# Optimization experiments

Hardware: AMD Instinct MI355X
Metric: run time of the kernel (lower is better)

## Reference

```python
import jax, jax.numpy as jnp
import numpy as np

B, S, IN, OUT, E, K = 4, 4096, 1024, 1024, 8, 2
SCALE = 512.0  # alpha / r = 512 / 1
TEMP = 1.0


def setup_inputs() -> dict:
    key = jax.random.key(0)
    k1, k2, k3, k4 = jax.random.split(key, 4)
    return {
        "x": jax.random.normal(k1, (B, S, IN), dtype=jnp.float32),
        "lora_A": jax.random.normal(k2, (E, 1, IN), dtype=jnp.float32) * 0.02,
        "lora_B": jax.random.normal(k3, (E, OUT, 1), dtype=jnp.float32) * 0.02,
        "gate_w": jax.random.normal(k4, (E, IN), dtype=jnp.float32) * 0.02,
        "gate_b": jnp.zeros((E,), dtype=jnp.float32),
    }


def reference(x, lora_A, lora_B, gate_w, gate_b):
    # segment-level gating: mean over seq, softmax over experts
    seg = x.mean(axis=1)                                    # [B, IN]
    logits = (seg @ gate_w.T + gate_b) / TEMP               # [B, E]
    gate_scores = jax.nn.softmax(logits, axis=-1)           # [B, E]
    topk_scores, topk_idx = jax.lax.top_k(gate_scores, K)   # [B, K] (same for all tokens in segment)

    # dense all-expert LoRA compute (eval mode: dropout is identity)
    h = jnp.einsum('bsi,eri->bser', x, lora_A)              # [B, S, E, r]
    expert_outputs = jnp.einsum('bser,eor->bseo', h, lora_B) * SCALE  # [B, S, E, OUT]

    # gather top-k experts per segment (broadcast over seq) and weighted-sum
    sel = jnp.take_along_axis(expert_outputs, topk_idx[:, None, :, None], axis=2)  # [B, S, K, OUT]
    out = jnp.sum(sel * topk_scores[:, None, :, None], axis=2)  # [B, S, OUT]
    return out
```

## Files before the change

### kernel.cpp

```cpp
#include <hip/hip_runtime.h>

#define SCALE_F 512.0f

#define WS_H     0
#define WS_GPART 131072

__global__ __launch_bounds__(256) void kA_h_gate(
    const float* __restrict__ x, const float* __restrict__ lora_A,
    const float* __restrict__ gate_w, float* __restrict__ h,
    float* __restrict__ gpart)
{
    const int tid  = threadIdx.x;
    const int w    = tid >> 6;
    const int lane = tid & 63;
    const int tok0 = blockIdx.x * 8;

    __shared__ float xbuf[8 * 1024];

    float4 W[4][4];
#pragma unroll
    for (int rr = 0; rr < 4; ++rr) {
        const int row = 4 * w + rr;
        const float* rp = (row < 8) ? (lora_A + row * 1024)
                                    : (gate_w + (row - 8) * 1024);
        const float4* rp4 = (const float4*)rp;
#pragma unroll
        for (int j = 0; j < 4; ++j) W[rr][j] = rp4[lane + 64 * j];
    }

    const float4* src = (const float4*)(x + (size_t)tok0 * 1024);
    float4* dst = (float4*)xbuf;
#pragma unroll
    for (int j = 0; j < 8; ++j) dst[tid + 256 * j] = src[tid + 256 * j];
    __syncthreads();

    float gacc[4] = {0.f, 0.f, 0.f, 0.f};

#pragma unroll 2
    for (int t = 0; t < 8; ++t) {
        const float4* xr = (const float4*)(xbuf + t * 1024);
        const float4 xv0 = xr[lane];
        const float4 xv1 = xr[lane + 64];
        const float4 xv2 = xr[lane + 128];
        const float4 xv3 = xr[lane + 192];

        float p[4];
#pragma unroll
        for (int rr = 0; rr < 4; ++rr) {
            const float4 a0 = W[rr][0], a1 = W[rr][1];
            const float4 a2 = W[rr][2], a3 = W[rr][3];
            float s;
            s  = xv0.x * a0.x + xv0.y * a0.y + xv0.z * a0.z + xv0.w * a0.w;
            s += xv1.x * a1.x + xv1.y * a1.y + xv1.z * a1.z + xv1.w * a1.w;
            s += xv2.x * a2.x + xv2.y * a2.y + xv2.z * a2.z + xv2.w * a2.w;
            s += xv3.x * a3.x + xv3.y * a3.y + xv3.z * a3.z + xv3.w * a3.w;
            p[rr] = s;
        }

        if (w < 2) {
#pragma unroll
            for (int off = 32; off > 0; off >>= 1) {
                p[0] += __shfl_xor(p[0], off);
                p[1] += __shfl_xor(p[1], off);
                p[2] += __shfl_xor(p[2], off);
                p[3] += __shfl_xor(p[3], off);
            }
            if (lane == 0) {
                float4 hv = make_float4(p[0], p[1], p[2], p[3]);
                *(float4*)(h + (size_t)(tok0 + t) * 8 + w * 4) = hv;
            }
        } else {
            gacc[0] += p[0]; gacc[1] += p[1]; gacc[2] += p[2]; gacc[3] += p[3];
        }
    }

    if (w >= 2) {
#pragma unroll
        for (int off = 32; off > 0; off >>= 1) {
            gacc[0] += __shfl_xor(gacc[0], off);
            gacc[1] += __shfl_xor(gacc[1], off);
            gacc[2] += __shfl_xor(gacc[2], off);
            gacc[3] += __shfl_xor(gacc[3], off);
        }
        if (lane == 0) {
            float4 gv = make_float4(gacc[0], gacc[1], gacc[2], gacc[3]);
            *(float4*)(gpart + (size_t)blockIdx.x * 8 + (w - 2) * 4) = gv;
        }
    }
}

static __device__ __forceinline__ float4 f4add(float4 a, float4 b) {
    return make_float4(a.x + b.x, a.y + b.y, a.z + b.z, a.w + b.w);
}

__global__ __launch_bounds__(256) void kB_gate_combine(
    const float* __restrict__ h, const float* __restrict__ gpart,
    const float* __restrict__ gate_b, const float* __restrict__ lora_B,
    float* __restrict__ out)
{
    const int tid  = threadIdx.x;
    const int blk  = blockIdx.x;
    const int b    = blk >> 9;
    const int tok0 = blk * 8;

    __shared__ float4 s4[256];
    __shared__ float  s_h[64];
    __shared__ float  s_logit[8];
    __shared__ int    s_sel[2];
    __shared__ float  s_coef[2];

    const float4* gp4 = (const float4*)(gpart + (size_t)b * 4096);
    float4 acc = gp4[tid];
    acc = f4add(acc, gp4[tid + 256]);
    acc = f4add(acc, gp4[tid + 512]);
    acc = f4add(acc, gp4[tid + 768]);
    s4[tid] = acc;

    if (tid < 64) s_h[tid] = h[(size_t)tok0 * 8 + tid];
    __syncthreads();

    if (tid < 64) {
        float4 a = f4add(f4add(s4[tid], s4[tid + 64]),
                         f4add(s4[tid + 128], s4[tid + 192]));
        s4[tid] = a;
    }
    __syncthreads();
    if (tid < 16) {
        float4 a = f4add(f4add(s4[tid], s4[tid + 16]),
                         f4add(s4[tid + 32], s4[tid + 48]));
        s4[tid] = a;
    }
    __syncthreads();
    if (tid < 2) {
        float4 a = s4[tid];
#pragma unroll
        for (int q = 2; q < 16; q += 2) a = f4add(a, s4[tid + q]);
        const float inv = 1.0f / 4096.0f;
        s_logit[tid * 4 + 0] = a.x * inv + gate_b[tid * 4 + 0];
        s_logit[tid * 4 + 1] = a.y * inv + gate_b[tid * 4 + 1];
        s_logit[tid * 4 + 2] = a.z * inv + gate_b[tid * 4 + 2];
        s_logit[tid * 4 + 3] = a.w * inv + gate_b[tid * 4 + 3];
    }
    __syncthreads();

    if (tid == 0) {
        float sc[8];
        float m = -1e30f;
#pragma unroll
        for (int q = 0; q < 8; ++q) { sc[q] = s_logit[q]; m = fmaxf(m, sc[q]); }
        float sum = 0.f;
#pragma unroll
        for (int q = 0; q < 8; ++q) { sc[q] = __expf(sc[q] - m); sum += sc[q]; }
        const float invs = 1.0f / sum;

        int i0 = 0;
#pragma unroll
        for (int q = 1; q < 8; ++q) if (sc[q] > sc[i0]) i0 = q;
        int i1 = (i0 == 0) ? 1 : 0;
#pragma unroll
        for (int q = 0; q < 8; ++q) if (q != i0 && sc[q] > sc[i1]) i1 = q;

        s_sel[0]  = i0;
        s_sel[1]  = i1;
        s_coef[0] = SCALE_F * sc[i0] * invs;
        s_coef[1] = SCALE_F * sc[i1] * invs;
    }
    __syncthreads();

    const int   i0 = s_sel[0];
    const int   i1 = s_sel[1];
    const float c0 = s_coef[0];
    const float c1 = s_coef[1];

    const float4 b0 = ((const float4*)(lora_B + i0 * 1024))[tid];
    const float4 b1 = ((const float4*)(lora_B + i1 * 1024))[tid];
    const float4 v0 = make_float4(c0 * b0.x, c0 * b0.y, c0 * b0.z, c0 * b0.w);
    const float4 v1 = make_float4(c1 * b1.x, c1 * b1.y, c1 * b1.z, c1 * b1.w);

    float4* out4 = (float4*)out;
#pragma unroll
    for (int t = 0; t < 8; ++t) {
        const float h0 = s_h[t * 8 + i0];
        const float h1 = s_h[t * 8 + i1];
        float4 r;
        r.x = h0 * v0.x + h1 * v1.x;
        r.y = h0 * v0.y + h1 * v1.y;
        r.z = h0 * v0.z + h1 * v1.z;
        r.w = h0 * v0.w + h1 * v1.w;
        out4[(size_t)(tok0 + t) * 256 + tid] = r;
    }
}

extern "C" void kernel_launch(void* const* d_in, const int* in_sizes, int n_in,
                              void* d_out, int out_size, void* d_ws, size_t ws_size,
                              hipStream_t stream) {
    const float* x      = (const float*)d_in[0];
    const float* lora_A = (const float*)d_in[1];
    const float* lora_B = (const float*)d_in[2];
    const float* gate_w = (const float*)d_in[3];
    const float* gate_b = (const float*)d_in[4];
    float* out = (float*)d_out;

    float* ws    = (float*)d_ws;
    float* h     = ws + WS_H;
    float* gpart = ws + WS_GPART;

    kA_h_gate<<<2048, 256, 0, stream>>>(x, lora_A, gate_w, h, gpart);
    kB_gate_combine<<<2048, 256, 0, stream>>>(h, gpart, gate_b, lora_B, out);
}
```

Measured before the change: 128.7 us.

## Fuse gating and combine into one cooperative kernel with grid sync

Merges the two kernels into one cooperative kernel of 1024 blocks, each handling two 8-token tiles. The per-token h values stay in shared memory and are never written to global memory. A grid-wide sync separates the gate-partial phase from the softmax/top-k/output phase. This removes one kernel launch and the h round trip, but adds the cost of a grid barrier and needs every block co-resident. If the cooperative launch fails, the code falls back to the original two kernels.

```diff
diff --git a/kernel.cpp b/kernel.cpp
--- a/kernel.cpp
+++ b/kernel.cpp
@@ -1,9 +1,202 @@
 #include <hip/hip_runtime.h>
+#include <hip/hip_cooperative_groups.h>
+
+namespace cg = cooperative_groups;
 
 #define SCALE_F 512.0f
 
 #define WS_H     0
 #define WS_GPART 131072
+
+static __device__ __forceinline__ float4 f4add(float4 a, float4 b) {
+    return make_float4(a.x + b.x, a.y + b.y, a.z + b.z, a.w + b.w);
+}
+
+__global__ __launch_bounds__(256, 4) void k_fused(
+    const float* __restrict__ x, const float* __restrict__ lora_A,
+    const float* __restrict__ gate_w, const float* __restrict__ gate_b,
+    const float* __restrict__ lora_B, float* __restrict__ gpart,
+    float* __restrict__ out)
+{
+    const int tid  = threadIdx.x;
+    const int w    = tid >> 6;
+    const int lane = tid & 63;
+
+    __shared__ __align__(16) float xbuf[8 * 1024];
+    __shared__ __align__(16) float s_h[2][64];
+    __shared__ float4 s4[256];
+    __shared__ float  s_logit[8];
+    __shared__ int    s_sel[2];
+    __shared__ float  s_coef[2];
+
+    float4 W[4][4];
+#pragma unroll
+    for (int rr = 0; rr < 4; ++rr) {
+        const int row = 4 * w + rr;
+        const float* rp = (row < 8) ? (lora_A + row * 1024)
+                                    : (gate_w + (row - 8) * 1024);
+        const float4* rp4 = (const float4*)rp;
+#pragma unroll
+        for (int j = 0; j < 4; ++j) W[rr][j] = rp4[lane + 64 * j];
+    }
+
+#pragma unroll
+    for (int ti = 0; ti < 2; ++ti) {
+        const int tile = blockIdx.x + ti * 1024;
+        const int tok0 = tile * 8;
+
+        if (ti) __syncthreads();
+
+        const float4* src = (const float4*)(x + (size_t)tok0 * 1024);
+        float4* dst = (float4*)xbuf;
+#pragma unroll
+        for (int j = 0; j < 8; ++j) dst[tid + 256 * j] = src[tid + 256 * j];
+        __syncthreads();
+
+        float gacc[4] = {0.f, 0.f, 0.f, 0.f};
+
+#pragma unroll 2
+        for (int t = 0; t < 8; ++t) {
+            const float4* xr = (const float4*)(xbuf + t * 1024);
+            const float4 xv0 = xr[lane];
+            const float4 xv1 = xr[lane + 64];
+            const float4 xv2 = xr[lane + 128];
+            const float4 xv3 = xr[lane + 192];
+
+            float p[4];
+#pragma unroll
+            for (int rr = 0; rr < 4; ++rr) {
+                const float4 a0 = W[rr][0], a1 = W[rr][1];
+                const float4 a2 = W[rr][2], a3 = W[rr][3];
+                float s;
+                s  = xv0.x * a0.x + xv0.y * a0.y + xv0.z * a0.z + xv0.w * a0.w;
+                s += xv1.x * a1.x + xv1.y * a1.y + xv1.z * a1.z + xv1.w * a1.w;
+                s += xv2.x * a2.x + xv2.y * a2.y + xv2.z * a2.z + xv2.w * a2.w;
+                s += xv3.x * a3.x + xv3.y * a3.y + xv3.z * a3.z + xv3.w * a3.w;
+                p[rr] = s;
+            }
+
+            if (w < 2) {
+#pragma unroll
+                for (int off = 32; off > 0; off >>= 1) {
+                    p[0] += __shfl_xor(p[0], off);
+                    p[1] += __shfl_xor(p[1], off);
+                    p[2] += __shfl_xor(p[2], off);
+                    p[3] += __shfl_xor(p[3], off);
+                }
+                if (lane == 0) {
+                    float4 hv = make_float4(p[0], p[1], p[2], p[3]);
+                    *(float4*)&s_h[ti][t * 8 + w * 4] = hv;
+                }
+            } else {
+                gacc[0] += p[0]; gacc[1] += p[1]; gacc[2] += p[2]; gacc[3] += p[3];
+            }
+        }
+
+        if (w >= 2) {
+#pragma unroll
+            for (int off = 32; off > 0; off >>= 1) {
+                gacc[0] += __shfl_xor(gacc[0], off);
+                gacc[1] += __shfl_xor(gacc[1], off);
+                gacc[2] += __shfl_xor(gacc[2], off);
+                gacc[3] += __shfl_xor(gacc[3], off);
+            }
+            if (lane == 0) {
+                float4 gv = make_float4(gacc[0], gacc[1], gacc[2], gacc[3]);
+                *(float4*)(gpart + (size_t)tile * 8 + (w - 2) * 4) = gv;
+            }
+        }
+    }
+
+    __threadfence();
+    cg::this_grid().sync();
+
+#pragma unroll
+    for (int ti = 0; ti < 2; ++ti) {
+        const int tile = blockIdx.x + ti * 1024;
+        const int tok0 = tile * 8;
+        const int b    = tile >> 9;
+
+        if (ti) __syncthreads();
+
+        const float4* gp4 = (const float4*)(gpart + (size_t)b * 4096);
+        float4 acc = gp4[tid];
+        acc = f4add(acc, gp4[tid + 256]);
+        acc = f4add(acc, gp4[tid + 512]);
+        acc = f4add(acc, gp4[tid + 768]);
+        s4[tid] = acc;
+        __syncthreads();
+
+        if (tid < 64) {
+            s4[tid] = f4add(f4add(s4[tid], s4[tid + 64]),
+                            f4add(s4[tid + 128], s4[tid + 192]));
+        }
+        __syncthreads();
+        if (tid < 16) {
+            s4[tid] = f4add(f4add(s4[tid], s4[tid + 16]),
+                            f4add(s4[tid + 32], s4[tid + 48]));
+        }
+        __syncthreads();
+        if (tid < 2) {
+            float4 a = s4[tid];
+#pragma unroll
+            for (int q = 2; q < 16; q += 2) a = f4add(a, s4[tid + q]);
+            const float inv = 1.0f / 4096.0f;
+            s_logit[tid * 4 + 0] = a.x * inv + gate_b[tid * 4 + 0];
+            s_logit[tid * 4 + 1] = a.y * inv + gate_b[tid * 4 + 1];
+            s_logit[tid * 4 + 2] = a.z * inv + gate_b[tid * 4 + 2];
+            s_logit[tid * 4 + 3] = a.w * inv + gate_b[tid * 4 + 3];
+        }
+        __syncthreads();
+
+        if (tid == 0) {
+            float sc[8];
+            float m = -1e30f;
+#pragma unroll
+            for (int q = 0; q < 8; ++q) { sc[q] = s_logit[q]; m = fmaxf(m, sc[q]); }
+            float sum = 0.f;
+#pragma unroll
+            for (int q = 0; q < 8; ++q) { sc[q] = __expf(sc[q] - m); sum += sc[q]; }
+            const float invs = 1.0f / sum;
+
+            int i0 = 0;
+#pragma unroll
+            for (int q = 1; q < 8; ++q) if (sc[q] > sc[i0]) i0 = q;
+            int i1 = (i0 == 0) ? 1 : 0;
+#pragma unroll
+            for (int q = 0; q < 8; ++q) if (q != i0 && sc[q] > sc[i1]) i1 = q;
+
+            s_sel[0]  = i0;
+            s_sel[1]  = i1;
+            s_coef[0] = SCALE_F * sc[i0] * invs;
+            s_coef[1] = SCALE_F * sc[i1] * invs;
+        }
+        __syncthreads();
+
+        const int   i0 = s_sel[0];
+        const int   i1 = s_sel[1];
+        const float c0 = s_coef[0];
+        const float c1 = s_coef[1];
+
+        const float4 b0 = ((const float4*)(lora_B + i0 * 1024))[tid];
+        const float4 b1 = ((const float4*)(lora_B + i1 * 1024))[tid];
+        const float4 v0 = make_float4(c0 * b0.x, c0 * b0.y, c0 * b0.z, c0 * b0.w);
+        const float4 v1 = make_float4(c1 * b1.x, c1 * b1.y, c1 * b1.z, c1 * b1.w);
+
+        float4* out4 = (float4*)out;
+#pragma unroll
+        for (int t = 0; t < 8; ++t) {
+            const float h0 = s_h[ti][t * 8 + i0];
+            const float h1 = s_h[ti][t * 8 + i1];
+            float4 r;
+            r.x = h0 * v0.x + h1 * v1.x;
+            r.y = h0 * v0.y + h1 * v1.y;
+            r.z = h0 * v0.z + h1 * v1.z;
+            r.w = h0 * v0.w + h1 * v1.w;
+            out4[(size_t)(tok0 + t) * 256 + tid] = r;
+        }
+    }
+}
 
 __global__ __launch_bounds__(256) void kA_h_gate(
     const float* __restrict__ x, const float* __restrict__ lora_A,
@@ -89,10 +282,6 @@
     }
 }
 
-static __device__ __forceinline__ float4 f4add(float4 a, float4 b) {
-    return make_float4(a.x + b.x, a.y + b.y, a.z + b.z, a.w + b.w);
-}
-
 __global__ __launch_bounds__(256) void kB_gate_combine(
     const float* __restrict__ h, const float* __restrict__ gpart,
     const float* __restrict__ gate_b, const float* __restrict__ lora_B,
@@ -120,15 +309,13 @@
     __syncthreads();
 
     if (tid < 64) {
-        float4 a = f4add(f4add(s4[tid], s4[tid + 64]),
-                         f4add(s4[tid + 128], s4[tid + 192]));
-        s4[tid] = a;
+        s4[tid] = f4add(f4add(s4[tid], s4[tid + 64]),
+                        f4add(s4[tid + 128], s4[tid + 192]));
     }
     __syncthreads();
     if (tid < 16) {
-        float4 a = f4add(f4add(s4[tid], s4[tid + 16]),
-                         f4add(s4[tid + 32], s4[tid + 48]));
-        s4[tid] = a;
+        s4[tid] = f4add(f4add(s4[tid], s4[tid + 16]),
+                        f4add(s4[tid + 32], s4[tid + 48]));
     }
     __syncthreads();
     if (tid < 2) {
@@ -205,6 +392,13 @@
     float* h     = ws + WS_H;
     float* gpart = ws + WS_GPART;
 
-    kA_h_gate<<<2048, 256, 0, stream>>>(x, lora_A, gate_w, h, gpart);
-    kB_gate_combine<<<2048, 256, 0, stream>>>(h, gpart, gate_b, lora_B, out);
+    void* args[] = {(void*)&x, (void*)&lora_A, (void*)&gate_w, (void*)&gate_b,
+                    (void*)&lora_B, (void*)&gpart, (void*)&out};
+    hipError_t err = hipLaunchCooperativeKernel((const void*)k_fused, dim3(1024),
+                                                dim3(256), args, 0, stream);
+    if (err != hipSuccess) {
+        (void)hipGetLastError();
+        kA_h_gate<<<2048, 256, 0, stream>>>(x, lora_A, gate_w, h, gpart);
+        kB_gate_combine<<<2048, 256, 0, stream>>>(h, gpart, gate_b, lora_B, out);
+    }
 }
```

Result: slower. 317.9 us (+146.9%).
